# Optimization experiments

Measured on AMD Instinct MI355X. Metric: run time of the kernel, lower is better.

## Reference

```python
import jax, jax.numpy as jnp
import numpy as np

LN_EPS = 1e-5


def _act_quant(x):
    # per-token int8 absmax quantization (BitNet style)
    s = 127.0 / jnp.clip(jnp.max(jnp.abs(x), axis=-1, keepdims=True), 1e-5)
    return jnp.clip(jnp.round(x * s), -128.0, 127.0) / s


def _weight_quant(w):
    # ternary 1.58-bit weight quantization with global mean-abs scale
    s = 1.0 / jnp.clip(jnp.mean(jnp.abs(w)), 1e-5)
    return jnp.clip(jnp.round(w * s), -1.0, 1.0) / s


def _ste(x, q):
    # straight-through estimator: forward uses q, gradient flows through x
    return x + jax.lax.stop_gradient(q - x)


def _bitlinear(x, w, b):
    xq = _ste(x, _act_quant(x))
    wq = _ste(w, _weight_quant(w))
    return jnp.einsum('bsd,hd->bsh', xq, wq) + b


def _layernorm(x, gamma, beta):
    mu = jnp.mean(x, axis=-1, keepdims=True)
    var = jnp.mean(jnp.square(x - mu), axis=-1, keepdims=True)
    return (x - mu) * jax.lax.rsqrt(var + LN_EPS) * gamma + beta


def setup_inputs() -> dict:
    key = jax.random.key(0)
    ks = jax.random.split(key, 3)
    B, S, D, H = 4, 4096, 2048, 8192
    return {
        'x': jax.random.normal(ks[0], (B, S, D), dtype=jnp.float32),
        'gamma': jnp.ones((D,), jnp.float32),
        'beta': jnp.zeros((D,), jnp.float32),
        'w1': jax.random.normal(ks[1], (H, D), jnp.float32) * (1.0 / np.sqrt(D)),
        'b1': jnp.zeros((H,), jnp.float32),
        'w2': jax.random.normal(ks[2], (D, H), jnp.float32) * (1.0 / np.sqrt(H)),
        'b2': jnp.zeros((D,), jnp.float32),
    }


def reference(x, gamma, beta, w1, b1, w2, b2):
    h = _layernorm(x, gamma, beta)
    h = _bitlinear(h, w1, b1)            # [B,S,H]
    h = jax.nn.gelu(h, approximate=False)  # torch nn.GELU default = exact erf
    out = _bitlinear(h, w2, b2)          # [B,S,D]
    return out
```

## Files before the change

kernel.cpp:

```cpp
#include <hip/hip_runtime.h>
#include <hip/hip_bf16.h>


typedef __attribute__((ext_vector_type(8))) short short8;
typedef __attribute__((ext_vector_type(4))) int int4v;

#define D_DIM 2048
#define H_DIM 8192
#define M_DIM 16384
#define MCHUNK 4096

__device__ __forceinline__ float block_sum(float v, float* buf) {
#pragma unroll
  for (int o = 32; o > 0; o >>= 1) v += __shfl_down(v, o, 64);
  const int lane = threadIdx.x & 63, w = threadIdx.x >> 6;
  if (lane == 0) buf[w] = v;
  __syncthreads();
  float r = buf[0] + buf[1] + buf[2] + buf[3];
  __syncthreads();
  return r;
}
__device__ __forceinline__ float block_max(float v, float* buf) {
#pragma unroll
  for (int o = 32; o > 0; o >>= 1) v = fmaxf(v, __shfl_down(v, o, 64));
  const int lane = threadIdx.x & 63, w = threadIdx.x >> 6;
  if (lane == 0) buf[w] = v;
  __syncthreads();
  float r = fmaxf(fmaxf(buf[0], buf[1]), fmaxf(buf[2], buf[3]));
  __syncthreads();
  return r;
}

__device__ __forceinline__ void lds16(const signed char* g, signed char* l) {
  __builtin_amdgcn_global_load_lds(
      (const __attribute__((address_space(1))) unsigned int*)g,
      (__attribute__((address_space(3))) unsigned int*)l, 16, 0, 0);
}

__global__ __launch_bounds__(256) void absmean_partial(const float* __restrict__ w,
                                                       int n, double* __restrict__ part) {
  __shared__ float buf[4];
  float s = 0.0f;
  const long stride = (long)gridDim.x * 256 * 4;
  for (long i = ((long)blockIdx.x * 256 + threadIdx.x) * 4; i < n; i += stride) {
    float4 v = *(const float4*)(w + i);
    s += fabsf(v.x) + fabsf(v.y) + fabsf(v.z) + fabsf(v.w);
  }
  float r = block_sum(s, buf);
  if (threadIdx.x == 0) part[blockIdx.x] = (double)r;
}

__global__ __launch_bounds__(256) void absmean_final(const double* __restrict__ part,
                                                     int nb, double n, double* __restrict__ out) {
  __shared__ double buf[4];
  double s = 0.0;
  for (int i = threadIdx.x; i < nb; i += 256) s += part[i];
#pragma unroll
  for (int o = 32; o > 0; o >>= 1) s += __shfl_down(s, o, 64);
  const int lane = threadIdx.x & 63, w = threadIdx.x >> 6;
  if (lane == 0) buf[w] = s;
  __syncthreads();
  if (threadIdx.x == 0) out[0] = (buf[0] + buf[1] + buf[2] + buf[3]) / n;
}

__global__ __launch_bounds__(256) void wquant_kernel(const float* __restrict__ w,
                                                     const double* __restrict__ mean,
                                                     signed char* __restrict__ wq, int n) {
  long i = ((long)blockIdx.x * 256 + threadIdx.x) * 4;
  if (i >= n) return;
  const float s = 1.0f / (float)fmax(mean[0], 1e-5);
  float4 v = *(const float4*)(w + i);
  __align__(4) signed char q[4];
  q[0] = (signed char)(int)fminf(fmaxf(rintf(v.x * s), -1.f), 1.f);
  q[1] = (signed char)(int)fminf(fmaxf(rintf(v.y * s), -1.f), 1.f);
  q[2] = (signed char)(int)fminf(fmaxf(rintf(v.z * s), -1.f), 1.f);
  q[3] = (signed char)(int)fminf(fmaxf(rintf(v.w * s), -1.f), 1.f);
  *(int*)(wq + i) = *(int*)q;
}

__global__ __launch_bounds__(256) void ln_quant_kernel(const float* __restrict__ x,
                                                       const float* __restrict__ gamma,
                                                       const float* __restrict__ beta,
                                                       signed char* __restrict__ aq,
                                                       float* __restrict__ ds) {
  __shared__ float buf[4];
  const int t = threadIdx.x;
  const long row = blockIdx.x;
  const float* xr = x + row * (long)D_DIM;
  float v[8];
  *(float4*)(v)     = *(const float4*)(xr + t * 8);
  *(float4*)(v + 4) = *(const float4*)(xr + t * 8 + 4);
  float s = 0.f;
#pragma unroll
  for (int i = 0; i < 8; ++i) s += v[i];
  s = block_sum(s, buf);
  const float mu = s * (1.0f / 2048.0f);
  float sq = 0.f;
#pragma unroll
  for (int i = 0; i < 8; ++i) { float d = v[i] - mu; sq += d * d; }
  sq = block_sum(sq, buf);
  const float inv = 1.0f / sqrtf(sq * (1.0f / 2048.0f) + 1e-5f);
  float gam[8], bet[8];
  *(float4*)(gam)     = *(const float4*)(gamma + t * 8);
  *(float4*)(gam + 4) = *(const float4*)(gamma + t * 8 + 4);
  *(float4*)(bet)     = *(const float4*)(beta + t * 8);
  *(float4*)(bet + 4) = *(const float4*)(beta + t * 8 + 4);
  float xn[8]; float am = 0.f;
#pragma unroll
  for (int i = 0; i < 8; ++i) {
    xn[i] = (v[i] - mu) * inv * gam[i] + bet[i];
    am = fmaxf(am, fabsf(xn[i]));
  }
  am = block_max(am, buf);
  am = fmaxf(am, 1e-5f);
  const float qs = 127.0f / am;
  __align__(8) signed char q[8];
#pragma unroll
  for (int i = 0; i < 8; ++i)
    q[i] = (signed char)(int)fminf(fmaxf(rintf(xn[i] * qs), -128.f), 127.f);
  *(long*)(aq + row * D_DIM + t * 8) = *(long*)q;
  if (t == 0) ds[row] = am / 127.0f;
}

__global__ __launch_bounds__(256) void hquant32_kernel(const float* __restrict__ src,
                                                       signed char* __restrict__ dst,
                                                       float* __restrict__ ds2) {
  __shared__ float buf[4];
  const int t = threadIdx.x;
  const long row = blockIdx.x;
  const float* sr = src + row * (long)H_DIM;
  float v[4][8];
#pragma unroll
  for (int c = 0; c < 4; ++c) {
    *(float4*)(v[c])     = *(const float4*)(sr + (c * 256 + t) * 8);
    *(float4*)(v[c] + 4) = *(const float4*)(sr + (c * 256 + t) * 8 + 4);
  }
  float am = 0.f;
#pragma unroll
  for (int c = 0; c < 4; ++c)
#pragma unroll
    for (int i = 0; i < 8; ++i) am = fmaxf(am, fabsf(v[c][i]));
  am = block_max(am, buf);
  am = fmaxf(am, 1e-5f);
  const float qs = 127.0f / am;
  signed char* dr = dst + row * (long)H_DIM;
#pragma unroll
  for (int c = 0; c < 4; ++c) {
    __align__(8) signed char o[8];
#pragma unroll
    for (int i = 0; i < 8; ++i)
      o[i] = (signed char)(int)fminf(fmaxf(rintf(v[c][i] * qs), -128.f), 127.f);
    *(long*)(dr + (c * 256 + t) * 8) = *(long*)o;
  }
  if (t == 0) ds2[row] = am / 127.0f;
}

__device__ __forceinline__ void read_a4(const signed char* sm, int base, int4v (&af)[4]) {
#pragma unroll
  for (int ms = 0; ms < 4; ++ms)
    af[ms] = *(const int4v*)&sm[base + ms * 1024];
}
__device__ __forceinline__ void read_b2(const signed char* sm, int base, int4v (&bf)[2]) {
#pragma unroll
  for (int ns = 0; ns < 2; ++ns)
    bf[ns] = *(const int4v*)&sm[base + ns * 1024];
}
__device__ __forceinline__ void mfma_q(const int4v (&af)[4], const int4v (&bf)[2],
                                       int4v (&acc)[8][4], int m0, int n0) {
#pragma unroll
  for (int ms = 0; ms < 4; ++ms)
#pragma unroll
    for (int ns = 0; ns < 2; ++ns)
      acc[m0 + ms][n0 + ns] = __builtin_amdgcn_mfma_i32_16x16x64_i8(
          af[ms], bf[ns], acc[m0 + ms][n0 + ns], 0, 0, 0);
}

template <int EPI>
__global__ __launch_bounds__(512, 2) void gemm256_kernel(
    const signed char* __restrict__ A,
    const signed char* __restrict__ Bm,
    const float* __restrict__ dsA,
    const double* __restrict__ meanw,
    const float* __restrict__ bias,
    float* __restrict__ outf,
    int NBX, int N, int K) {
  __shared__ __align__(16) signed char smA[2 * 256 * 64];
  __shared__ __align__(16) signed char smB[2 * 256 * 64];
  const int tid = threadIdx.x;
  const int lane = tid & 63;
  const int wid = tid >> 6;
  const int wr = wid >> 2;
  const int wcn = wid & 3;

  const int cpx = gridDim.x >> 3;
  const int swz = ((int)blockIdx.x & 7) * cpx + ((int)blockIdx.x >> 3);
  const int bx = swz % NBX, by = swz / NBX;
  const long r0 = (long)by * 256;
  const long c0 = (long)bx * 256;

  const int srow = tid >> 2;
  const int schunk = (tid & 3) ^ (srow & 3) ^ ((srow >> 2) & 3);
  const signed char* gAs = A + (r0 + srow) * (long)K + schunk * 16;
  const signed char* gBs = Bm + (c0 + srow) * (long)K + schunk * 16;

  const int frow = lane & 15;
  const int fchunk = (lane >> 4) ^ (frow & 3) ^ ((frow >> 2) & 3);
  const int fbyte = frow * 64 + fchunk * 16;
  const int baseA = wr * 8192 + fbyte;
  const int baseB = (wcn >> 1) * 8192 + (wcn & 1) * 4096 + fbyte;

  int4v acc[8][4] = {};
  int4v af[4], bf0[2], bf1[2];
  const int nk = K >> 6;
  const int nk2 = nk >> 1;

#define STG(gbase, h, t, smbase, d)                                           \
    lds16((gbase) + (long)((h) * 128) * K + (long)(t) * 64,                   \
          &(smbase)[(d) * 16384 + (h) * 8192 + tid * 16]);
#define BAR  __builtin_amdgcn_s_barrier()
#define SCB  __builtin_amdgcn_sched_barrier(0)
#define LGKM0 asm volatile("s_waitcnt lgkmcnt(0)" ::: "memory")
#define PRIO1 __builtin_amdgcn_s_setprio(1)
#define PRIO0 __builtin_amdgcn_s_setprio(0)

  STG(gAs, 0, 0, smA, 0); STG(gAs, 1, 0, smA, 0);
  STG(gBs, 0, 0, smB, 0); STG(gBs, 1, 0, smB, 0);
  STG(gAs, 0, 1, smA, 1);
  asm volatile("s_waitcnt vmcnt(1)" ::: "memory");
  SCB; BAR; SCB;

  for (int i = 0; i < nk2; ++i) {
    const int t1 = 2 * i + 1;
    const int tn0 = 2 * i + 2;
    const int tn1 = 2 * i + 3;
    const bool s0 = tn0 < nk, s1 = tn1 < nk;

    read_a4(smA, baseA, af);
    read_b2(smB, baseB, bf0);
    STG(gAs, 1, t1, smA, 1);
    SCB; BAR; LGKM0; SCB;
    PRIO1; mfma_q(af, bf0, acc, 0, 0); PRIO0;
    SCB; BAR;

    read_b2(smB, baseB + 2048, bf1);
    STG(gBs, 0, t1, smB, 1);
    SCB; BAR; LGKM0; SCB;
    PRIO1; mfma_q(af, bf1, acc, 0, 2); PRIO0;
    SCB; BAR;

    read_a4(smA, baseA + 4096, af);
    STG(gBs, 1, t1, smB, 1);
    SCB; BAR; LGKM0; SCB;
    PRIO1; mfma_q(af, bf1, acc, 4, 2); PRIO0;
    SCB; BAR;

    if (s0) STG(gAs, 0, tn0, smA, 0);
    SCB; BAR; SCB;
    PRIO1; mfma_q(af, bf0, acc, 4, 0); PRIO0;
    SCB;
    if (s0) { asm volatile("s_waitcnt vmcnt(1)" ::: "memory"); }
    else    { asm volatile("s_waitcnt vmcnt(0)" ::: "memory"); }
    SCB; BAR;

    read_a4(smA, 16384 + baseA, af);
    read_b2(smB, 16384 + baseB, bf0);
    if (s0) STG(gAs, 1, tn0, smA, 0);
    SCB; BAR; LGKM0; SCB;
    PRIO1; mfma_q(af, bf0, acc, 0, 0); PRIO0;
    SCB; BAR;

    read_b2(smB, 16384 + baseB + 2048, bf1);
    if (s0) STG(gBs, 0, tn0, smB, 0);
    SCB; BAR; LGKM0; SCB;
    PRIO1; mfma_q(af, bf1, acc, 0, 2); PRIO0;
    SCB; BAR;

    read_a4(smA, 16384 + baseA + 4096, af);
    if (s0) STG(gBs, 1, tn0, smB, 0);
    SCB; BAR; LGKM0; SCB;
    PRIO1; mfma_q(af, bf1, acc, 4, 2); PRIO0;
    SCB; BAR;

    if (s1) STG(gAs, 0, tn1, smA, 1);
    SCB; BAR; SCB;
    PRIO1; mfma_q(af, bf0, acc, 4, 0); PRIO0;
    SCB;
    if (s1) { asm volatile("s_waitcnt vmcnt(1)" ::: "memory"); }
    else    { asm volatile("s_waitcnt vmcnt(0)" ::: "memory"); }
    SCB; BAR;
  }
#undef STG
#undef BAR
#undef SCB
#undef LGKM0
#undef PRIO1
#undef PRIO0

  const float sw = (float)fmax(meanw[0], 1e-5);
#pragma unroll
  for (int m = 0; m < 8; ++m) {
#pragma unroll
    for (int j = 0; j < 4; ++j) {
      const long row = r0 + wr * 128 + m * 16 + (lane >> 4) * 4 + j;
      const float sa = dsA[row] * sw;
#pragma unroll
      for (int n = 0; n < 4; ++n) {
        const long col = c0 + wcn * 64 + n * 16 + (lane & 15);
        float v = (float)acc[m][n][j] * sa + bias[col];
        if (EPI == 1) {
          float gl = 0.5f * v * (1.0f + erff(v * 0.70710678118654752f));
          outf[row * (long)N + col] = gl;
        } else {
          outf[row * (long)N + col] = v;
        }
      }
    }
  }
}

extern "C" void kernel_launch(void* const* d_in, const int* in_sizes, int n_in,
                              void* d_out, int out_size, void* d_ws, size_t ws_size,
                              hipStream_t stream) {
  const float* x     = (const float*)d_in[0];
  const float* gamma = (const float*)d_in[1];
  const float* beta  = (const float*)d_in[2];
  const float* w1    = (const float*)d_in[3];
  const float* b1    = (const float*)d_in[4];
  const float* w2    = (const float*)d_in[5];
  const float* b2    = (const float*)d_in[6];

  char* ws = (char*)d_ws;
  double* part1 = (double*)(ws + 0);
  double* part2 = (double*)(ws + 16384);
  double* means = (double*)(ws + 32768);
  float* ds1  = (float*)(ws + 65536);
  float* ds2  = (float*)(ws + 131072);
  signed char* wq = (signed char*)(ws + 1048576l);
  signed char* aq = (signed char*)(ws + 17825792l);
  signed char* hq = (signed char*)(ws + 51380224l);

  const int NW = 16777216;
  float* hstage = (float*)d_out;

  absmean_partial<<<2048, 256, 0, stream>>>(w1, NW, part1);
  absmean_partial<<<2048, 256, 0, stream>>>(w2, NW, part2);
  absmean_final<<<1, 256, 0, stream>>>(part1, 2048, (double)NW, means + 0);
  absmean_final<<<1, 256, 0, stream>>>(part2, 2048, (double)NW, means + 1);
  wquant_kernel<<<16384, 256, 0, stream>>>(w1, means + 0, wq, NW);
  ln_quant_kernel<<<16384, 256, 0, stream>>>(x, gamma, beta, aq, ds1);

  for (int c = 0; c < 4; ++c) {
    const long r0 = (long)c * MCHUNK;
    gemm256_kernel<1><<<(H_DIM / 256) * (MCHUNK / 256), 512, 0, stream>>>(
        aq + r0 * D_DIM, wq, ds1 + r0, means + 0, b1, hstage,
        H_DIM / 256, H_DIM, D_DIM);
    hquant32_kernel<<<MCHUNK, 256, 0, stream>>>(
        hstage, hq + r0 * H_DIM, ds2 + r0);
  }

  wquant_kernel<<<16384, 256, 0, stream>>>(w2, means + 1, wq, NW);

  gemm256_kernel<2><<<(D_DIM / 256) * (M_DIM / 256), 512, 0, stream>>>(
      hq, wq, ds2, means + 1, b2, (float*)d_out,
      D_DIM / 256, D_DIM, H_DIM);
}
```

Baseline: 989.5 us.

## Use fragment-ordered LDS staging layout and halve barriers in int8 GEMM loop

```diff
diff --git a/kernel.cpp b/kernel.cpp
--- a/kernel.cpp
+++ b/kernel.cpp
@@ -2,7 +2,6 @@
 #include <hip/hip_bf16.h>
 
 
-typedef __attribute__((ext_vector_type(8))) short short8;
 typedef __attribute__((ext_vector_type(4))) int int4v;
 
 #define D_DIM 2048
@@ -198,16 +197,13 @@
   const long r0 = (long)by * 256;
   const long c0 = (long)bx * 256;
 
-  const int srow = tid >> 2;
-  const int schunk = (tid & 3) ^ (srow & 3) ^ ((srow >> 2) & 3);
+  const int srow = ((tid >> 6) << 4) + (tid & 15);
+  const int schunk = (tid >> 4) & 3;
   const signed char* gAs = A + (r0 + srow) * (long)K + schunk * 16;
   const signed char* gBs = Bm + (c0 + srow) * (long)K + schunk * 16;
 
-  const int frow = lane & 15;
-  const int fchunk = (lane >> 4) ^ (frow & 3) ^ ((frow >> 2) & 3);
-  const int fbyte = frow * 64 + fchunk * 16;
-  const int baseA = wr * 8192 + fbyte;
-  const int baseB = (wcn >> 1) * 8192 + (wcn & 1) * 4096 + fbyte;
+  const int baseA = wr * 8192 + lane * 16;
+  const int baseB = (wcn >> 1) * 8192 + (wcn & 1) * 4096 + lane * 16;
 
   int4v acc[8][4] = {};
   int4v af[4], bf0[2], bf1[2];
@@ -238,56 +234,56 @@
     read_a4(smA, baseA, af);
     read_b2(smB, baseB, bf0);
     STG(gAs, 1, t1, smA, 1);
-    SCB; BAR; LGKM0; SCB;
+    LGKM0; SCB;
     PRIO1; mfma_q(af, bf0, acc, 0, 0); PRIO0;
-    SCB; BAR;
+    SCB; BAR; SCB;
 
     read_b2(smB, baseB + 2048, bf1);
     STG(gBs, 0, t1, smB, 1);
-    SCB; BAR; LGKM0; SCB;
+    LGKM0; SCB;
     PRIO1; mfma_q(af, bf1, acc, 0, 2); PRIO0;
-    SCB; BAR;
+    SCB; BAR; SCB;
 
     read_a4(smA, baseA + 4096, af);
     STG(gBs, 1, t1, smB, 1);
-    SCB; BAR; LGKM0; SCB;
+    LGKM0; SCB;
     PRIO1; mfma_q(af, bf1, acc, 4, 2); PRIO0;
-    SCB; BAR;
+    SCB; BAR; SCB;
 
     if (s0) STG(gAs, 0, tn0, smA, 0);
-    SCB; BAR; SCB;
+    SCB;
     PRIO1; mfma_q(af, bf0, acc, 4, 0); PRIO0;
     SCB;
     if (s0) { asm volatile("s_waitcnt vmcnt(1)" ::: "memory"); }
     else    { asm volatile("s_waitcnt vmcnt(0)" ::: "memory"); }
-    SCB; BAR;
+    SCB; BAR; SCB;
 
     read_a4(smA, 16384 + baseA, af);
     read_b2(smB, 16384 + baseB, bf0);
     if (s0) STG(gAs, 1, tn0, smA, 0);
-    SCB; BAR; LGKM0; SCB;
+    LGKM0; SCB;
     PRIO1; mfma_q(af, bf0, acc, 0, 0); PRIO0;
-    SCB; BAR;
+    SCB; BAR; SCB;
 
     read_b2(smB, 16384 + baseB + 2048, bf1);
     if (s0) STG(gBs, 0, tn0, smB, 0);
-    SCB; BAR; LGKM0; SCB;
+    LGKM0; SCB;
     PRIO1; mfma_q(af, bf1, acc, 0, 2); PRIO0;
-    SCB; BAR;
+    SCB; BAR; SCB;
 
     read_a4(smA, 16384 + baseA + 4096, af);
     if (s0) STG(gBs, 1, tn0, smB, 0);
-    SCB; BAR; LGKM0; SCB;
+    LGKM0; SCB;
     PRIO1; mfma_q(af, bf1, acc, 4, 2); PRIO0;
-    SCB; BAR;
+    SCB; BAR; SCB;
 
     if (s1) STG(gAs, 0, tn1, smA, 1);
-    SCB; BAR; SCB;
+    SCB;
     PRIO1; mfma_q(af, bf0, acc, 4, 0); PRIO0;
     SCB;
     if (s1) { asm volatile("s_waitcnt vmcnt(1)" ::: "memory"); }
     else    { asm volatile("s_waitcnt vmcnt(0)" ::: "memory"); }
-    SCB; BAR;
+    SCB; BAR; SCB;
   }
 #undef STG
 #undef BAR
```

Result: slower. 1.063 ms (+7.4%).

## Shrink GEMM block tile to 256x128 with four waves per block

Applied to the files above, without the earlier changes.

```diff
diff --git a/kernel.cpp b/kernel.cpp
--- a/kernel.cpp
+++ b/kernel.cpp
@@ -2,7 +2,6 @@
 #include <hip/hip_bf16.h>
 
 
-typedef __attribute__((ext_vector_type(8))) short short8;
 typedef __attribute__((ext_vector_type(4))) int int4v;
 
 #define D_DIM 2048
@@ -176,7 +175,7 @@
 }
 
 template <int EPI>
-__global__ __launch_bounds__(512, 2) void gemm256_kernel(
+__global__ __launch_bounds__(256, 2) void gemm256_kernel(
     const signed char* __restrict__ A,
     const signed char* __restrict__ Bm,
     const float* __restrict__ dsA,
@@ -185,48 +184,55 @@
     float* __restrict__ outf,
     int NBX, int N, int K) {
   __shared__ __align__(16) signed char smA[2 * 256 * 64];
-  __shared__ __align__(16) signed char smB[2 * 256 * 64];
+  __shared__ __align__(16) signed char smB[2 * 128 * 64];
   const int tid = threadIdx.x;
   const int lane = tid & 63;
-  const int wid = tid >> 6;
-  const int wr = wid >> 2;
-  const int wcn = wid & 3;
+  const int wv = tid >> 6;
+  const int wr = wv >> 1;
+  const int wcn = wv & 1;
 
   const int cpx = gridDim.x >> 3;
   const int swz = ((int)blockIdx.x & 7) * cpx + ((int)blockIdx.x >> 3);
   const int bx = swz % NBX, by = swz / NBX;
   const long r0 = (long)by * 256;
-  const long c0 = (long)bx * 256;
-
-  const int srow = tid >> 2;
-  const int schunk = (tid & 3) ^ (srow & 3) ^ ((srow >> 2) & 3);
-  const signed char* gAs = A + (r0 + srow) * (long)K + schunk * 16;
-  const signed char* gBs = Bm + (c0 + srow) * (long)K + schunk * 16;
+  const long c0 = (long)bx * 128;
+
+  const int srw = wv * 32 + (lane >> 2);
+  const int sch = (lane & 3) ^ ((lane >> 2) & 3) ^ ((lane >> 4) & 3);
+  const signed char* gAs = A + (r0 + srw) * (long)K + sch * 16;
+  const signed char* gBs = Bm + (c0 + srw) * (long)K + sch * 16;
+  const int wbase = wv * 2048;
 
   const int frow = lane & 15;
   const int fchunk = (lane >> 4) ^ (frow & 3) ^ ((frow >> 2) & 3);
   const int fbyte = frow * 64 + fchunk * 16;
   const int baseA = wr * 8192 + fbyte;
-  const int baseB = (wcn >> 1) * 8192 + (wcn & 1) * 4096 + fbyte;
+  const int baseB = wcn * 4096 + fbyte;
 
   int4v acc[8][4] = {};
   int4v af[4], bf0[2], bf1[2];
   const int nk = K >> 6;
   const int nk2 = nk >> 1;
 
-#define STG(gbase, h, t, smbase, d)                                           \
-    lds16((gbase) + (long)((h) * 128) * K + (long)(t) * 64,                   \
-          &(smbase)[(d) * 16384 + (h) * 8192 + tid * 16]);
+#define STGA(h, t, d) {                                                        \
+    lds16(gAs + (long)((h) * 128) * K + (long)(t) * 64,                        \
+          &smA[(d) * 16384 + (h) * 8192 + wbase + lane * 16]);                 \
+    lds16(gAs + (long)((h) * 128 + 16) * K + (long)(t) * 64,                   \
+          &smA[(d) * 16384 + (h) * 8192 + wbase + 1024 + lane * 16]); }
+#define STGB(t, d) {                                                           \
+    lds16(gBs + (long)(t) * 64,                                                \
+          &smB[(d) * 8192 + wbase + lane * 16]);                               \
+    lds16(gBs + (long)16 * K + (long)(t) * 64,                                 \
+          &smB[(d) * 8192 + wbase + 1024 + lane * 16]); }
 #define BAR  __builtin_amdgcn_s_barrier()
 #define SCB  __builtin_amdgcn_sched_barrier(0)
 #define LGKM0 asm volatile("s_waitcnt lgkmcnt(0)" ::: "memory")
 #define PRIO1 __builtin_amdgcn_s_setprio(1)
 #define PRIO0 __builtin_amdgcn_s_setprio(0)
 
-  STG(gAs, 0, 0, smA, 0); STG(gAs, 1, 0, smA, 0);
-  STG(gBs, 0, 0, smB, 0); STG(gBs, 1, 0, smB, 0);
-  STG(gAs, 0, 1, smA, 1);
-  asm volatile("s_waitcnt vmcnt(1)" ::: "memory");
+  STGA(0, 0, 0); STGA(1, 0, 0); STGB(0, 0);
+  STGA(0, 1, 1);
+  asm volatile("s_waitcnt vmcnt(2)" ::: "memory");
   SCB; BAR; SCB;
 
   for (int i = 0; i < nk2; ++i) {
@@ -237,59 +243,58 @@
 
     read_a4(smA, baseA, af);
     read_b2(smB, baseB, bf0);
-    STG(gAs, 1, t1, smA, 1);
+    STGA(1, t1, 1);
     SCB; BAR; LGKM0; SCB;
     PRIO1; mfma_q(af, bf0, acc, 0, 0); PRIO0;
     SCB; BAR;
 
     read_b2(smB, baseB + 2048, bf1);
-    STG(gBs, 0, t1, smB, 1);
+    STGB(t1, 1);
     SCB; BAR; LGKM0; SCB;
     PRIO1; mfma_q(af, bf1, acc, 0, 2); PRIO0;
     SCB; BAR;
 
     read_a4(smA, baseA + 4096, af);
-    STG(gBs, 1, t1, smB, 1);
     SCB; BAR; LGKM0; SCB;
     PRIO1; mfma_q(af, bf1, acc, 4, 2); PRIO0;
     SCB; BAR;
 
-    if (s0) STG(gAs, 0, tn0, smA, 0);
+    if (s0) STGA(0, tn0, 0);
     SCB; BAR; SCB;
     PRIO1; mfma_q(af, bf0, acc, 4, 0); PRIO0;
     SCB;
-    if (s0) { asm volatile("s_waitcnt vmcnt(1)" ::: "memory"); }
+    if (s0) { asm volatile("s_waitcnt vmcnt(2)" ::: "memory"); }
     else    { asm volatile("s_waitcnt vmcnt(0)" ::: "memory"); }
     SCB; BAR;
 
     read_a4(smA, 16384 + baseA, af);
-    read_b2(smB, 16384 + baseB, bf0);
-    if (s0) STG(gAs, 1, tn0, smA, 0);
+    read_b2(smB, 8192 + baseB, bf0);
+    if (s0) STGA(1, tn0, 0);
     SCB; BAR; LGKM0; SCB;
     PRIO1; mfma_q(af, bf0, acc, 0, 0); PRIO0;
     SCB; BAR;
 
-    read_b2(smB, 16384 + baseB + 2048, bf1);
-    if (s0) STG(gBs, 0, tn0, smB, 0);
+    read_b2(smB, 8192 + baseB + 2048, bf1);
+    if (s0) STGB(tn0, 0);
     SCB; BAR; LGKM0; SCB;
     PRIO1; mfma_q(af, bf1, acc, 0, 2); PRIO0;
     SCB; BAR;
 
     read_a4(smA, 16384 + baseA + 4096, af);
-    if (s0) STG(gBs, 1, tn0, smB, 0);
     SCB; BAR; LGKM0; SCB;
     PRIO1; mfma_q(af, bf1, acc, 4, 2); PRIO0;
     SCB; BAR;
 
-    if (s1) STG(gAs, 0, tn1, smA, 1);
+    if (s1) STGA(0, tn1, 1);
     SCB; BAR; SCB;
     PRIO1; mfma_q(af, bf0, acc, 4, 0); PRIO0;
     SCB;
-    if (s1) { asm volatile("s_waitcnt vmcnt(1)" ::: "memory"); }
+    if (s1) { asm volatile("s_waitcnt vmcnt(2)" ::: "memory"); }
     else    { asm volatile("s_waitcnt vmcnt(0)" ::: "memory"); }
     SCB; BAR;
   }
-#undef STG
+#undef STGA
+#undef STGB
 #undef BAR
 #undef SCB
 #undef LGKM0
@@ -351,16 +356,16 @@
 
   for (int c = 0; c < 4; ++c) {
     const long r0 = (long)c * MCHUNK;
-    gemm256_kernel<1><<<(H_DIM / 256) * (MCHUNK / 256), 512, 0, stream>>>(
+    gemm256_kernel<1><<<(H_DIM / 128) * (MCHUNK / 256), 256, 0, stream>>>(
         aq + r0 * D_DIM, wq, ds1 + r0, means + 0, b1, hstage,
-        H_DIM / 256, H_DIM, D_DIM);
+        H_DIM / 128, H_DIM, D_DIM);
     hquant32_kernel<<<MCHUNK, 256, 0, stream>>>(
         hstage, hq + r0 * H_DIM, ds2 + r0);
   }
 
   wquant_kernel<<<16384, 256, 0, stream>>>(w2, means + 1, wq, NW);
 
-  gemm256_kernel<2><<<(D_DIM / 256) * (M_DIM / 256), 512, 0, stream>>>(
+  gemm256_kernel<2><<<(D_DIM / 128) * (M_DIM / 256), 256, 0, stream>>>(
       hq, wq, ds2, means + 1, b2, (float*)d_out,
-      D_DIM / 256, D_DIM, H_DIM);
-}
+      D_DIM / 128, D_DIM, H_DIM);
+}
```

Measured after the change: 1.108 ms. +11.9%, slower.

## Restructure int8 GEMM main loop into simple double-buffered pipeline with fewer barriers

Applied to the files above, without the earlier changes.

```diff
diff --git a/kernel.cpp b/kernel.cpp
--- a/kernel.cpp
+++ b/kernel.cpp
@@ -2,7 +2,6 @@
 #include <hip/hip_bf16.h>
 
 
-typedef __attribute__((ext_vector_type(8))) short short8;
 typedef __attribute__((ext_vector_type(4))) int int4v;
 
 #define D_DIM 2048
@@ -210,89 +209,51 @@
   const int baseB = (wcn >> 1) * 8192 + (wcn & 1) * 4096 + fbyte;
 
   int4v acc[8][4] = {};
-  int4v af[4], bf0[2], bf1[2];
+  int4v afLo[4], afHi[4], bf0[2], bf1[2];
   const int nk = K >> 6;
-  const int nk2 = nk >> 1;
 
 #define STG(gbase, h, t, smbase, d)                                           \
     lds16((gbase) + (long)((h) * 128) * K + (long)(t) * 64,                   \
           &(smbase)[(d) * 16384 + (h) * 8192 + tid * 16]);
 #define BAR  __builtin_amdgcn_s_barrier()
 #define SCB  __builtin_amdgcn_sched_barrier(0)
-#define LGKM0 asm volatile("s_waitcnt lgkmcnt(0)" ::: "memory")
 #define PRIO1 __builtin_amdgcn_s_setprio(1)
 #define PRIO0 __builtin_amdgcn_s_setprio(0)
 
   STG(gAs, 0, 0, smA, 0); STG(gAs, 1, 0, smA, 0);
   STG(gBs, 0, 0, smB, 0); STG(gBs, 1, 0, smB, 0);
-  STG(gAs, 0, 1, smA, 1);
-  asm volatile("s_waitcnt vmcnt(1)" ::: "memory");
+  STG(gAs, 0, 1, smA, 1); STG(gAs, 1, 1, smA, 1);
+  STG(gBs, 0, 1, smB, 1); STG(gBs, 1, 1, smB, 1);
+  asm volatile("s_waitcnt vmcnt(4)" ::: "memory");
   SCB; BAR; SCB;
 
-  for (int i = 0; i < nk2; ++i) {
-    const int t1 = 2 * i + 1;
-    const int tn0 = 2 * i + 2;
-    const int tn1 = 2 * i + 3;
-    const bool s0 = tn0 < nk, s1 = tn1 < nk;
-
-    read_a4(smA, baseA, af);
-    read_b2(smB, baseB, bf0);
-    STG(gAs, 1, t1, smA, 1);
-    SCB; BAR; LGKM0; SCB;
-    PRIO1; mfma_q(af, bf0, acc, 0, 0); PRIO0;
-    SCB; BAR;
-
-    read_b2(smB, baseB + 2048, bf1);
-    STG(gBs, 0, t1, smB, 1);
-    SCB; BAR; LGKM0; SCB;
-    PRIO1; mfma_q(af, bf1, acc, 0, 2); PRIO0;
-    SCB; BAR;
-
-    read_a4(smA, baseA + 4096, af);
-    STG(gBs, 1, t1, smB, 1);
-    SCB; BAR; LGKM0; SCB;
-    PRIO1; mfma_q(af, bf1, acc, 4, 2); PRIO0;
-    SCB; BAR;
-
-    if (s0) STG(gAs, 0, tn0, smA, 0);
-    SCB; BAR; SCB;
-    PRIO1; mfma_q(af, bf0, acc, 4, 0); PRIO0;
+  for (int t = 0; t < nk; ++t) {
+    const int c = t & 1;
+    const int off = c * 16384;
+
+    read_a4(smA, off + baseA, afLo);
+    read_b2(smB, off + baseB, bf0);
+    read_b2(smB, off + baseB + 2048, bf1);
+    read_a4(smA, off + baseA + 4096, afHi);
     SCB;
-    if (s0) { asm volatile("s_waitcnt vmcnt(1)" ::: "memory"); }
-    else    { asm volatile("s_waitcnt vmcnt(0)" ::: "memory"); }
-    SCB; BAR;
-
-    read_a4(smA, 16384 + baseA, af);
-    read_b2(smB, 16384 + baseB, bf0);
-    if (s0) STG(gAs, 1, tn0, smA, 0);
-    SCB; BAR; LGKM0; SCB;
-    PRIO1; mfma_q(af, bf0, acc, 0, 0); PRIO0;
-    SCB; BAR;
-
-    read_b2(smB, 16384 + baseB + 2048, bf1);
-    if (s0) STG(gBs, 0, tn0, smB, 0);
-    SCB; BAR; LGKM0; SCB;
-    PRIO1; mfma_q(af, bf1, acc, 0, 2); PRIO0;
-    SCB; BAR;
-
-    read_a4(smA, 16384 + baseA + 4096, af);
-    if (s0) STG(gBs, 1, tn0, smB, 0);
-    SCB; BAR; LGKM0; SCB;
-    PRIO1; mfma_q(af, bf1, acc, 4, 2); PRIO0;
-    SCB; BAR;
-
-    if (s1) STG(gAs, 0, tn1, smA, 1);
-    SCB; BAR; SCB;
-    PRIO1; mfma_q(af, bf0, acc, 4, 0); PRIO0;
-    SCB;
-    if (s1) { asm volatile("s_waitcnt vmcnt(1)" ::: "memory"); }
-    else    { asm volatile("s_waitcnt vmcnt(0)" ::: "memory"); }
-    SCB; BAR;
+    asm volatile("s_waitcnt lgkmcnt(6)" ::: "memory"); SCB;
+    PRIO1; mfma_q(afLo, bf0, acc, 0, 0); PRIO0; SCB;
+    asm volatile("s_waitcnt lgkmcnt(4)" ::: "memory"); SCB;
+    PRIO1; mfma_q(afLo, bf1, acc, 0, 2); PRIO0; SCB;
+    asm volatile("s_waitcnt lgkmcnt(0)" ::: "memory"); SCB;
+    PRIO1; mfma_q(afHi, bf1, acc, 4, 2); mfma_q(afHi, bf0, acc, 4, 0); PRIO0; SCB;
+
+    asm volatile("s_waitcnt vmcnt(0)" ::: "memory"); SCB;
+    BAR; SCB;
+
+    if (t + 2 < nk) {
+      STG(gAs, 0, t + 2, smA, c); STG(gAs, 1, t + 2, smA, c);
+      STG(gBs, 0, t + 2, smB, c); STG(gBs, 1, t + 2, smB, c);
+    }
   }
 #undef STG
 #undef BAR
 #undef SCB
-#undef LGKM0
 #undef PRIO1
 #undef PRIO0
 
```

After: 1.094 ms. 1.11x slower.
